# Kernel tuning notes

Hardware: AMD Instinct MI355X
Metric: run time of the kernel (lower is better)

The kernel has to match this reference:

```python
import jax, jax.numpy as jnp
import numpy as np
import math

D_MODEL = 1024
N_HEAD = 16


def setup_inputs() -> dict:
    key = jax.random.key(0)
    k1, k2, k3 = jax.random.split(key, 3)
    B, S, E = 2, 2048, D_MODEL
    x = jax.random.normal(k1, (B, S, E), dtype=jnp.float32)
    # Linear weights stored as (in, out); init scaled like typical transformer init
    w_attn = jax.random.normal(k2, (E, 3 * E), dtype=jnp.float32) * (1.0 / math.sqrt(E))
    w_proj = jax.random.normal(k3, (E, E), dtype=jnp.float32) * (1.0 / math.sqrt(E))
    return {"x": x, "w_attn": w_attn, "w_proj": w_proj}


def reference(x, w_attn, w_proj):
    B, S, E = x.shape
    H = N_HEAD
    Dh = E // H
    qkv = x @ w_attn  # (B, S, 3E)
    q, k, v = jnp.split(qkv, 3, axis=-1)
    # (B, H, S, Dh)
    q = q.reshape(B, S, H, Dh).transpose(0, 2, 1, 3)
    k = k.reshape(B, S, H, Dh).transpose(0, 2, 1, 3)
    v = v.reshape(B, S, H, Dh).transpose(0, 2, 1, 3)
    scale = 1.0 / math.sqrt(Dh)
    att = jnp.einsum('bhqd,bhkd->bhqk', q, k) * scale  # (B, H, S, S)
    causal = jnp.tril(jnp.ones((S, S), dtype=bool))
    att = jnp.where(causal, att, -jnp.inf)
    att = jax.nn.softmax(att, axis=-1)
    # dropout = 0.0 (eval mode) -> identity
    y = jnp.einsum('bhqk,bhkd->bhqd', att, v)  # (B, H, S, Dh)
    y = y.transpose(0, 2, 1, 3).reshape(B, S, E)
    return y @ w_proj
```

## Files before the change

### kernel.cpp

```cpp
#include <hip/hip_runtime.h>
#include <hip/hip_bf16.h>

#define S_LEN 2048
#define EMB   1024
#define NH    16
#define DH    64
#define QKV_LD 3072

typedef __attribute__((ext_vector_type(8)))  __bf16 bf16x8;
typedef __attribute__((ext_vector_type(4)))  __bf16 bf16x4;
typedef __attribute__((ext_vector_type(4)))  float  f32x4;
typedef __attribute__((ext_vector_type(16))) float  f32x16;
typedef __attribute__((ext_vector_type(2)))  unsigned int u32x2;

__device__ __forceinline__ void gl_lds16(const void* g, void* l) {
  __builtin_amdgcn_global_load_lds(
      (const __attribute__((address_space(1))) void*)g,
      (__attribute__((address_space(3))) void*)l,
      16, 0, 0);
}

__global__ __launch_bounds__(256)
void prep_fused(const float* __restrict__ x, __bf16* __restrict__ xb,
                const float* __restrict__ w_attn, __bf16* __restrict__ wat,
                const float* __restrict__ w_proj, __bf16* __restrict__ wpt,
                int n8) {
  __shared__ float T[64][65];
  const int bid = blockIdx.x;
  const int tid = threadIdx.x;

  if (bid < 2048) {
    int i = bid * 256 + tid;
    if (i >= n8) return;
    const f32x4* p = (const f32x4*)(x + (size_t)i * 8);
    f32x4 a = p[0], b = p[1];
    bf16x8 o;
    #pragma unroll
    for (int j = 0; j < 4; j++) { o[j] = (__bf16)a[j]; o[4 + j] = (__bf16)b[j]; }
    *(bf16x8*)(xb + (size_t)i * 8) = o;
    return;
  }

  const float* W; __bf16* Wt; int K, N, k0, n0;
  if (bid < 2048 + 768) {
    int t = bid - 2048;
    W = w_attn; Wt = wat; K = 1024; N = 3072;
    n0 = (t % 48) * 64; k0 = (t / 48) * 64;
  } else {
    int t = bid - 2816;
    W = w_proj; Wt = wpt; K = 1024; N = 1024;
    n0 = (t & 15) * 64; k0 = (t >> 4) * 64;
  }
  #pragma unroll
  for (int t = 0; t < 16; t++) {
    int idx = tid + t * 256;
    int r = idx >> 6, c = idx & 63;
    T[r][c] = W[(size_t)(k0 + r) * N + n0 + c];
  }
  __syncthreads();
  #pragma unroll
  for (int t = 0; t < 16; t++) {
    int idx = tid + t * 256;
    int r = idx >> 6, c = idx & 63;
    Wt[(size_t)(n0 + r) * K + k0 + c] = (__bf16)T[c][r];
  }
}

#define TM 128
#define TK 32

template <typename OutT, int TNv>
__global__ __launch_bounds__(256, 2)
void gemm_bf16_mfma(const __bf16* __restrict__ A, const __bf16* __restrict__ Bt,
                    OutT* __restrict__ C, int M, int N, int K) {
  __shared__ __align__(16) __bf16 As[2][TM][TK];
  __shared__ __align__(16) __bf16 Bs[2][TNv][TK];
  const int tid  = threadIdx.x;
  const int lane = tid & 63;
  const int w    = tid >> 6;
  const int wr   = w >> 1, wc = w & 1;
  const int brow = blockIdx.y * TM;
  const int bcol = blockIdx.x * TNv;
  const int l15  = lane & 15;
  const int grp  = lane >> 4;

  constexpr int NBI = TNv / 64;
  constexpr int WCT = TNv / 2;
  constexpr int NN  = WCT / 16;

  auto stage = [&](int k0, int buf) {
    #pragma unroll
    for (int j = 0; j < 2; j++) {
      const int cid = w * 128 + j * 64 + lane;
      const int row = cid >> 2, k8 = (cid & 3) * 8;
      gl_lds16(A + (size_t)(brow + row) * K + k0 + k8,
               &As[buf][0][0] + (size_t)(w * 128 + j * 64) * 8);
    }
    #pragma unroll
    for (int j = 0; j < NBI; j++) {
      const int cid = (w * NBI + j) * 64 + lane;
      const int row = cid >> 2, k8 = (cid & 3) * 8;
      gl_lds16(Bt + (size_t)(bcol + row) * K + k0 + k8,
               &Bs[buf][0][0] + (size_t)((w * NBI + j) * 64) * 8);
    }
  };

  f32x4 acc[4][NN];
  #pragma unroll
  for (int m = 0; m < 4; m++)
    #pragma unroll
    for (int n = 0; n < NN; n++) acc[m][n] = (f32x4){0.f, 0.f, 0.f, 0.f};

  stage(0, 0);
  __syncthreads();

  const int nk = K / TK;
  for (int kt = 0; kt < nk; kt++) {
    const int cur = kt & 1;
    if (kt + 1 < nk) stage((kt + 1) * TK, cur ^ 1);

    bf16x8 a[4], b[NN];
    #pragma unroll
    for (int m = 0; m < 4; m++)
      a[m] = *(const bf16x8*)&As[cur][wr * 64 + m * 16 + l15][grp * 8];
    #pragma unroll
    for (int n = 0; n < NN; n++)
      b[n] = *(const bf16x8*)&Bs[cur][wc * WCT + n * 16 + l15][grp * 8];
    #pragma unroll
    for (int m = 0; m < 4; m++)
      #pragma unroll
      for (int n = 0; n < NN; n++)
        acc[m][n] = __builtin_amdgcn_mfma_f32_16x16x32_bf16(a[m], b[n], acc[m][n], 0, 0, 0);

    __syncthreads();
  }

  #pragma unroll
  for (int m = 0; m < 4; m++)
    #pragma unroll
    for (int r = 0; r < 4; r++) {
      const size_t row = (size_t)(brow + wr * 64 + m * 16 + grp * 4 + r);
      #pragma unroll
      for (int n = 0; n < NN; n++)
        C[row * N + bcol + wc * WCT + n * 16 + l15] = (OutT)acc[m][n][r];
    }
}

#define QB 64
#define KB 64
#define QSCALE 0.18033688f

__device__ __constant__ unsigned char ITEMS[44] = {
  76, 72, 68, 64,
  125, 127, 121, 60,
  123, 117, 119, 113, 56,
  115, 109, 111, 105, 52,
  107, 101, 103, 97, 48,
  99, 93, 95, 89, 44,
  91, 85, 87, 81, 40,
  83, 36,
  32, 28, 24, 20, 16, 12, 8, 4, 0
};

__global__ __launch_bounds__(256, 4)
void attn_mfma(const __bf16* __restrict__ qkv, __bf16* __restrict__ y,
               float* __restrict__ pO, float* __restrict__ pml) {
  __shared__ __align__(16) __bf16 Ks[2][KB][64];
  __shared__ __align__(16) __bf16 Vs[2][4096];

  const int tid  = threadIdx.x;
  const int lane = tid & 63;
  const int w    = tid >> 6;

  const int bid = blockIdx.x;
  const int xcd = bid & 7;
  const int j   = bid >> 3;
  const int g   = xcd * 4 + j / 44;
  const int idx = j % 44;

  const int code  = ITEMS[idx];
  const bool split = code & 1;
  const int khalf = (code >> 1) & 1;
  const int qtile = code >> 2;

  int it0, it1;
  bool diag;
  if (!split) {
    it0 = 0; it1 = qtile + 1; diag = true;
  } else {
    const int half = (qtile + 2) >> 1;
    it0 = khalf ? half : 0;
    it1 = khalf ? qtile + 1 : half;
    diag = (khalf == 1);
  }
  const int h = g & 15, b = g >> 4;
  const int pidx = split ? ((g * 12 + (qtile - 20)) * 2 + khalf) : 0;

  const __bf16* base = qkv + (size_t)b * S_LEN * QKV_LD;

  const int l31 = lane & 31;
  const int hl  = lane >> 5;
  const int qh  = w >> 1;
  const int kh  = w & 1;

  const int voff32 = ((lane >> 4) & 1) * 2048 + hl * 128 + (lane & 15) * 8
                   + kh * 1024;

  auto stageK = [&](int j0, int buf) {
    #pragma unroll
    for (int jj = 0; jj < 2; jj++) {
      const int cid = w * 128 + jj * 64 + lane;
      const int r = cid >> 3, pc = cid & 7;
      const int lc = pc ^ (r & 7);
      gl_lds16(base + (size_t)(j0 + r) * QKV_LD + EMB + h * DH + lc * 8,
               (char*)&Ks[buf][0][0] + (w * 128 + jj * 64) * 16);
    }
  };
  auto stageV = [&](int j0, int buf) {
    #pragma unroll
    for (int jj = 0; jj < 2; jj++) {
      const int cid = w * 128 + jj * 64 + lane;
      const int db = cid >> 7, sk = (cid >> 3) & 15;
      const int jr = (cid >> 1) & 3, ch = cid & 1;
      gl_lds16(base + (size_t)(j0 + sk * 4 + jr) * QKV_LD + 2 * EMB + h * DH
                    + db * 16 + ch * 8,
               (char*)&Vs[buf][0] + (w * 128 + jj * 64) * 16);
    }
  };

  const int qbase = qtile * QB;
  const int q = qbase + qh * 32 + l31;

  bf16x8 qf[4];
  {
    const __bf16* qp = base + (size_t)q * QKV_LD + h * DH;
    #pragma unroll
    for (int dq = 0; dq < 4; dq++) {
      bf16x8 v = *(const bf16x8*)(qp + dq * 16 + hl * 8);
      #pragma unroll
      for (int i2 = 0; i2 < 8; i2++) qf[dq][i2] = (__bf16)((float)v[i2] * QSCALE);
    }
  }

  f32x16 o_acc[2];
  #pragma unroll
  for (int d2 = 0; d2 < 2; d2++)
    #pragma unroll
    for (int r = 0; r < 16; r++) o_acc[d2][r] = 0.f;
  float m = -1e30f, l = 0.f;

  auto process = [&](int cur, int j0, bool masked) {
    f32x16 s;
    #pragma unroll
    for (int r = 0; r < 16; r++) s[r] = 0.f;
    const int krow = kh * 32 + l31;
    __builtin_amdgcn_s_setprio(1);
    #pragma unroll
    for (int dq = 0; dq < 4; dq++) {
      bf16x8 kf = *(const bf16x8*)&Ks[cur][krow][((dq * 2 + hl) ^ (krow & 7)) * 8];
      s = __builtin_amdgcn_mfma_f32_32x32x16_bf16(kf, qf[dq], s, 0, 0, 0);
    }
    __builtin_amdgcn_s_setprio(0);

    if (masked) {
      const int lim = q - j0 - kh * 32 - 4 * hl;
      #pragma unroll
      for (int r = 0; r < 16; r++) {
        const int kl = (r & 3) + 8 * (r >> 2);
        if (kl > lim) s[r] = -2e30f;
      }
    }

    float tmax = s[0];
    #pragma unroll
    for (int r = 1; r < 16; r++) tmax = fmaxf(tmax, s[r]);
    tmax = fmaxf(tmax, __shfl_xor(tmax, 32));

    const bool grow = !__all(tmax <= m + 8.0f);
    float corr = 1.f;
    if (grow) {
      const float mnew = fmaxf(m, tmax);
      corr = __builtin_amdgcn_exp2f(m - mnew);
      m = mnew;
    }

    const unsigned vb =
        (unsigned)(uintptr_t)(__attribute__((address_space(3))) char*)(&Vs[cur][0])
        + (unsigned)voff32;
    u32x2 tv[8];
    asm volatile("ds_read_b64_tr_b16 %0, %1 offset:0"    : "=v"(tv[0]) : "v"(vb));
    asm volatile("ds_read_b64_tr_b16 %0, %1 offset:256"  : "=v"(tv[1]) : "v"(vb));
    asm volatile("ds_read_b64_tr_b16 %0, %1 offset:512"  : "=v"(tv[2]) : "v"(vb));
    asm volatile("ds_read_b64_tr_b16 %0, %1 offset:768"  : "=v"(tv[3]) : "v"(vb));
    asm volatile("ds_read_b64_tr_b16 %0, %1 offset:4096" : "=v"(tv[4]) : "v"(vb));
    asm volatile("ds_read_b64_tr_b16 %0, %1 offset:4352" : "=v"(tv[5]) : "v"(vb));
    asm volatile("ds_read_b64_tr_b16 %0, %1 offset:4608" : "=v"(tv[6]) : "v"(vb));
    asm volatile("ds_read_b64_tr_b16 %0, %1 offset:4864" : "=v"(tv[7]) : "v"(vb));

    float psum = 0.f;
    #pragma unroll
    for (int r = 0; r < 16; r++) {
      float p = __builtin_amdgcn_exp2f(s[r] - m);
      s[r] = p;
      psum += p;
    }

    bf16x8 pb0, pb1;
    #pragma unroll
    for (int i2 = 0; i2 < 8; i2++) {
      pb0[i2] = (__bf16)s[i2];
      pb1[i2] = (__bf16)s[8 + i2];
    }

    if (grow) {
      #pragma unroll
      for (int d2 = 0; d2 < 2; d2++)
        #pragma unroll
        for (int r = 0; r < 16; r++) o_acc[d2][r] *= corr;
    }

    asm volatile("s_waitcnt lgkmcnt(0)");
    __builtin_amdgcn_sched_barrier(0);
    __builtin_amdgcn_s_setprio(1);
    #pragma unroll
    for (int d2 = 0; d2 < 2; d2++) {
      bf16x8 a0, a1;
      ((u32x2*)&a0)[0] = tv[d2 * 4 + 0]; ((u32x2*)&a0)[1] = tv[d2 * 4 + 1];
      ((u32x2*)&a1)[0] = tv[d2 * 4 + 2]; ((u32x2*)&a1)[1] = tv[d2 * 4 + 3];
      o_acc[d2] = __builtin_amdgcn_mfma_f32_32x32x16_bf16(a0, pb0, o_acc[d2], 0, 0, 0);
      o_acc[d2] = __builtin_amdgcn_mfma_f32_32x32x16_bf16(a1, pb1, o_acc[d2], 0, 0, 0);
    }
    __builtin_amdgcn_s_setprio(0);

    psum += __shfl_xor(psum, 32);
    l = grow ? (l * corr + psum) : (l + psum);
  };

  stageK(it0 * KB, 0);
  stageV(it0 * KB, 0);
  __syncthreads();

  const int nt = it1 - it0;
  #pragma unroll 1
  for (int tt = 0; tt < nt - 1; tt++) {
    const int cur = tt & 1;
    stageK((it0 + tt + 1) * KB, cur ^ 1);
    stageV((it0 + tt + 1) * KB, cur ^ 1);
    process(cur, (it0 + tt) * KB, false);
    __syncthreads();
  }

  process((nt - 1) & 1, (it1 - 1) * KB, diag);

  __syncthreads();
  float* exO  = (float*)&Vs[0][0];
  float* exML = (float*)&Ks[0][0][0];
  const int slot = qh * 64 + lane;
  if (kh) {
    #pragma unroll
    for (int r = 0; r < 16; r++) {
      exO[r * 128 + slot]        = o_acc[0][r];
      exO[(16 + r) * 128 + slot] = o_acc[1][r];
    }
    exML[slot]       = m;
    exML[128 + slot] = l;
  }
  __syncthreads();
  if (!kh) {
    const float m1  = exML[slot];
    const float l1v = exML[128 + slot];
    const float mm = fmaxf(m, m1);
    const float c0 = __builtin_amdgcn_exp2f(m - mm);
    const float c1 = __builtin_amdgcn_exp2f(m1 - mm);
    const float lsum = l * c0 + l1v * c1;
    if (split) {
      float* prow = pO + (size_t)pidx * 4096 + (size_t)(qh * 32 + l31) * 64;
      #pragma unroll
      for (int d2 = 0; d2 < 2; d2++)
        #pragma unroll
        for (int rq = 0; rq < 4; rq++) {
          f32x4 o4;
          #pragma unroll
          for (int jj = 0; jj < 4; jj++) {
            const int r = rq * 4 + jj;
            o4[jj] = o_acc[d2][r] * c0 + exO[(d2 * 16 + r) * 128 + slot] * c1;
          }
          *(f32x4*)&prow[d2 * 32 + rq * 8 + hl * 4] = o4;
        }
      if (!hl) {
        pml[(size_t)pidx * 128 + qh * 32 + l31]      = mm;
        pml[(size_t)pidx * 128 + 64 + qh * 32 + l31] = lsum;
      }
    } else {
      const float inv = 1.f / lsum;
      __bf16* yrow = y + ((size_t)(b * S_LEN + q)) * EMB + h * DH;
      #pragma unroll
      for (int d2 = 0; d2 < 2; d2++)
        #pragma unroll
        for (int rq = 0; rq < 4; rq++) {
          bf16x4 o4;
          #pragma unroll
          for (int jj = 0; jj < 4; jj++) {
            const int r = rq * 4 + jj;
            float v = (o_acc[d2][r] * c0 + exO[(d2 * 16 + r) * 128 + slot] * c1) * inv;
            o4[jj] = (__bf16)v;
          }
          *(bf16x4*)&yrow[d2 * 32 + rq * 8 + hl * 4] = o4;
        }
    }
  }
}

__global__ __launch_bounds__(256)
void attn_merge(const float* __restrict__ pO, const float* __restrict__ pml,
                __bf16* __restrict__ y) {
  const int mid = blockIdx.x;
  const int g = mid / 12, qrel = mid % 12;
  const int qt = 20 + qrel;
  const int b = g >> 4, h = g & 15;
  const int p0 = (g * 12 + qrel) * 2, p1 = p0 + 1;
  const int row = threadIdx.x >> 2;
  const int d0  = (threadIdx.x & 3) * 16;

  const float mA = pml[(size_t)p0 * 128 + row];
  const float lA = pml[(size_t)p0 * 128 + 64 + row];
  const float mB = pml[(size_t)p1 * 128 + row];
  const float lB = pml[(size_t)p1 * 128 + 64 + row];
  const float mm = fmaxf(mA, mB);
  const float cA = __builtin_amdgcn_exp2f(mA - mm);
  const float cB = __builtin_amdgcn_exp2f(mB - mm);
  const float inv = 1.f / (lA * cA + lB * cB);

  const float* OA = pO + (size_t)p0 * 4096 + (size_t)row * 64 + d0;
  const float* OB = pO + (size_t)p1 * 4096 + (size_t)row * 64 + d0;
  __bf16* yr = y + ((size_t)(b * S_LEN + qt * 64 + row)) * EMB + h * DH + d0;
  #pragma unroll
  for (int i = 0; i < 4; i++) {
    f32x4 va = *(const f32x4*)(OA + i * 4);
    f32x4 vb = *(const f32x4*)(OB + i * 4);
    bf16x4 o;
    #pragma unroll
    for (int jj = 0; jj < 4; jj++)
      o[jj] = (__bf16)((va[jj] * cA + vb[jj] * cB) * inv);
    *(bf16x4*)(yr + i * 4) = o;
  }
}

extern "C" void kernel_launch(void* const* d_in, const int* in_sizes, int n_in,
                              void* d_out, int out_size, void* d_ws, size_t ws_size,
                              hipStream_t stream) {
  const float* x      = (const float*)d_in[0];
  const float* w_attn = (const float*)d_in[1];
  const float* w_proj = (const float*)d_in[2];
  float* out = (float*)d_out;

  const int B = in_sizes[0] / (S_LEN * EMB);
  const int M = B * S_LEN;

  __bf16* xb   = (__bf16*)d_ws;
  __bf16* wat  = xb  + (size_t)M * EMB;
  __bf16* wpt  = wat + (size_t)QKV_LD * EMB;
  __bf16* qkvb = wpt + (size_t)EMB * EMB;
  __bf16* yb   = qkvb + (size_t)M * QKV_LD;

  float* pO  = (float*)d_ws;
  float* pml = pO + (size_t)768 * 4096;

  {
    int n8 = (M * EMB) / 8;
    prep_fused<<<dim3(3072), 256, 0, stream>>>(x, xb, w_attn, wat, w_proj, wpt, n8);
  }

  dim3 g1(QKV_LD / 128, M / TM);
  gemm_bf16_mfma<__bf16, 128><<<g1, 256, 0, stream>>>(xb, wat, qkvb, M, QKV_LD, EMB);

  attn_mfma<<<dim3(1408), 256, 0, stream>>>(qkvb, yb, pO, pml);
  attn_merge<<<dim3(384), 256, 0, stream>>>(pO, pml, yb);

  dim3 g3(EMB / 64, M / TM);
  gemm_bf16_mfma<float, 64><<<g3, 256, 0, stream>>>(yb, wpt, out, M, EMB, EMB);
}
```

Baseline: 111.1 us.

## Triple-buffer K/V tiles with vmcnt waits and split QK accumulation chains

Moves the K/V staging from double to triple buffering. Tiles are now prefetched two iterations ahead, and each iteration waits only on the older tile's loads through s_waitcnt vmcnt(4) and a bare s_barrier instead of a full __syncthreads. The QK^T MFMA chain is split into two independent accumulators so the four MFMAs are not serially dependent. The max and exp reductions are rewritten as trees to shorten dependency chains. LDS use rises by half, which may limit the 4 blocks per CU occupancy target, and the vmcnt(4) count assumes exactly 4 global loads per stage.

```diff
diff --git a/kernel.cpp b/kernel.cpp
--- a/kernel.cpp
+++ b/kernel.cpp
@@ -165,8 +165,8 @@
 __global__ __launch_bounds__(256, 4)
 void attn_mfma(const __bf16* __restrict__ qkv, __bf16* __restrict__ y,
                float* __restrict__ pO, float* __restrict__ pml) {
-  __shared__ __align__(16) __bf16 Ks[2][KB][64];
-  __shared__ __align__(16) __bf16 Vs[2][4096];
+  __shared__ __align__(16) __bf16 Ks[3][KB][64];
+  __shared__ __align__(16) __bf16 Vs[3][4096];
 
   const int tid  = threadIdx.x;
   const int lane = tid & 63;
@@ -250,39 +250,20 @@
   float m = -1e30f, l = 0.f;
 
   auto process = [&](int cur, int j0, bool masked) {
-    f32x16 s;
-    #pragma unroll
-    for (int r = 0; r < 16; r++) s[r] = 0.f;
+    f32x16 s, s2;
+    #pragma unroll
+    for (int r = 0; r < 16; r++) { s[r] = 0.f; s2[r] = 0.f; }
     const int krow = kh * 32 + l31;
+    bf16x8 kf0 = *(const bf16x8*)&Ks[cur][krow][((0 + hl) ^ (krow & 7)) * 8];
+    bf16x8 kf1 = *(const bf16x8*)&Ks[cur][krow][((2 + hl) ^ (krow & 7)) * 8];
+    bf16x8 kf2 = *(const bf16x8*)&Ks[cur][krow][((4 + hl) ^ (krow & 7)) * 8];
+    bf16x8 kf3 = *(const bf16x8*)&Ks[cur][krow][((6 + hl) ^ (krow & 7)) * 8];
     __builtin_amdgcn_s_setprio(1);
-    #pragma unroll
-    for (int dq = 0; dq < 4; dq++) {
-      bf16x8 kf = *(const bf16x8*)&Ks[cur][krow][((dq * 2 + hl) ^ (krow & 7)) * 8];
-      s = __builtin_amdgcn_mfma_f32_32x32x16_bf16(kf, qf[dq], s, 0, 0, 0);
-    }
+    s  = __builtin_amdgcn_mfma_f32_32x32x16_bf16(kf0, qf[0], s,  0, 0, 0);
+    s2 = __builtin_amdgcn_mfma_f32_32x32x16_bf16(kf1, qf[1], s2, 0, 0, 0);
+    s  = __builtin_amdgcn_mfma_f32_32x32x16_bf16(kf2, qf[2], s,  0, 0, 0);
+    s2 = __builtin_amdgcn_mfma_f32_32x32x16_bf16(kf3, qf[3], s2, 0, 0, 0);
     __builtin_amdgcn_s_setprio(0);
-
-    if (masked) {
-      const int lim = q - j0 - kh * 32 - 4 * hl;
-      #pragma unroll
-      for (int r = 0; r < 16; r++) {
-        const int kl = (r & 3) + 8 * (r >> 2);
-        if (kl > lim) s[r] = -2e30f;
-      }
-    }
-
-    float tmax = s[0];
-    #pragma unroll
-    for (int r = 1; r < 16; r++) tmax = fmaxf(tmax, s[r]);
-    tmax = fmaxf(tmax, __shfl_xor(tmax, 32));
-
-    const bool grow = !__all(tmax <= m + 8.0f);
-    float corr = 1.f;
-    if (grow) {
-      const float mnew = fmaxf(m, tmax);
-      corr = __builtin_amdgcn_exp2f(m - mnew);
-      m = mnew;
-    }
 
     const unsigned vb =
         (unsigned)(uintptr_t)(__attribute__((address_space(3))) char*)(&Vs[cur][0])
@@ -297,13 +278,47 @@
     asm volatile("ds_read_b64_tr_b16 %0, %1 offset:4608" : "=v"(tv[6]) : "v"(vb));
     asm volatile("ds_read_b64_tr_b16 %0, %1 offset:4864" : "=v"(tv[7]) : "v"(vb));
 
-    float psum = 0.f;
-    #pragma unroll
-    for (int r = 0; r < 16; r++) {
-      float p = __builtin_amdgcn_exp2f(s[r] - m);
-      s[r] = p;
-      psum += p;
-    }
+    #pragma unroll
+    for (int r = 0; r < 16; r++) s[r] += s2[r];
+
+    if (masked) {
+      const int lim = q - j0 - kh * 32 - 4 * hl;
+      #pragma unroll
+      for (int r = 0; r < 16; r++) {
+        const int kl = (r & 3) + 8 * (r >> 2);
+        if (kl > lim) s[r] = -2e30f;
+      }
+    }
+
+    float x0 = fmaxf(s[0], s[8]),  x1 = fmaxf(s[1], s[9]);
+    float x2 = fmaxf(s[2], s[10]), x3 = fmaxf(s[3], s[11]);
+    float x4 = fmaxf(s[4], s[12]), x5 = fmaxf(s[5], s[13]);
+    float x6 = fmaxf(s[6], s[14]), x7 = fmaxf(s[7], s[15]);
+    x0 = fmaxf(x0, x4); x1 = fmaxf(x1, x5);
+    x2 = fmaxf(x2, x6); x3 = fmaxf(x3, x7);
+    x0 = fmaxf(x0, x2); x1 = fmaxf(x1, x3);
+    float tmax = fmaxf(x0, x1);
+    tmax = fmaxf(tmax, __shfl_xor(tmax, 32));
+
+    const bool grow = !__all(tmax <= m + 8.0f);
+    float corr = 1.f;
+    if (grow) {
+      const float mnew = fmaxf(m, tmax);
+      corr = __builtin_amdgcn_exp2f(m - mnew);
+      m = mnew;
+    }
+
+    float ps0 = 0.f, ps1 = 0.f, ps2 = 0.f, ps3 = 0.f;
+    #pragma unroll
+    for (int r = 0; r < 16; r += 4) {
+      float p0 = __builtin_amdgcn_exp2f(s[r]     - m);
+      float p1 = __builtin_amdgcn_exp2f(s[r + 1] - m);
+      float p2 = __builtin_amdgcn_exp2f(s[r + 2] - m);
+      float p3 = __builtin_amdgcn_exp2f(s[r + 3] - m);
+      s[r] = p0; s[r + 1] = p1; s[r + 2] = p2; s[r + 3] = p3;
+      ps0 += p0; ps1 += p1; ps2 += p2; ps3 += p3;
+    }
+    float psum = (ps0 + ps1) + (ps2 + ps3);
 
     bf16x8 pb0, pb1;
     #pragma unroll
@@ -336,21 +351,26 @@
     l = grow ? (l * corr + psum) : (l + psum);
   };
 
+  const int nt = it1 - it0;
   stageK(it0 * KB, 0);
   stageV(it0 * KB, 0);
-  __syncthreads();
-
-  const int nt = it1 - it0;
+  if (nt > 1) { stageK((it0 + 1) * KB, 1); stageV((it0 + 1) * KB, 1); }
+
+  int cur = 0;
   #pragma unroll 1
-  for (int tt = 0; tt < nt - 1; tt++) {
-    const int cur = tt & 1;
-    stageK((it0 + tt + 1) * KB, cur ^ 1);
-    stageV((it0 + tt + 1) * KB, cur ^ 1);
-    process(cur, (it0 + tt) * KB, false);
-    __syncthreads();
-  }
-
-  process((nt - 1) & 1, (it1 - 1) * KB, diag);
+  for (int tt = 0; tt < nt; tt++) {
+    if (tt < nt - 1) asm volatile("s_waitcnt vmcnt(4)" ::: "memory");
+    else             asm volatile("s_waitcnt vmcnt(0)" ::: "memory");
+    __builtin_amdgcn_s_barrier();
+    __builtin_amdgcn_sched_barrier(0);
+    if (tt + 2 < nt) {
+      int nb = cur + 2; if (nb >= 3) nb -= 3;
+      stageK((it0 + tt + 2) * KB, nb);
+      stageV((it0 + tt + 2) * KB, nb);
+    }
+    process(cur, (it0 + tt) * KB, (tt == nt - 1) && diag);
+    cur = (cur == 2) ? 0 : cur + 1;
+  }
 
   __syncthreads();
   float* exO  = (float*)&Vs[0][0];
```

Measured after the change: 127.0 us. 1.14x slower.
